# Kernel tuning notes

Hardware: AMD Instinct MI355X
Metric: run time of the kernel (lower is better)

## Reference

```python
import jax, jax.numpy as jnp
import numpy as np
from jax import lax

N_SECTIONS, N_CHANNELS = 8, 128
KT, KF = 32, 16                 # kernel (time, freq)
LPOST = 400                     # section_length_postsyn
LPRE = KT + LPOST - 1           # 431, section_length_presyn
SECTION_DISTANCE = 400          # LPRE - overlap (overlap = 31)
N_TIMESTEPS, FREQ = 3231, 256
THRESHOLD = 15.0


def setup_inputs() -> dict:
    key = jax.random.key(0)
    k1, k2 = jax.random.split(key)
    # scale so mean conv response ~ threshold (512 taps * 0.8 * mean(X))
    X = jax.random.uniform(k1, (N_TIMESTEPS, FREQ), dtype=jnp.float32) * 0.073
    # SpykeTorch Convolution init: N(0.8, 0.05)
    W = 0.8 + 0.05 * jax.random.normal(k2, (N_SECTIONS, N_CHANNELS, 1, KT, KF), dtype=jnp.float32)
    return {"X": X, "W": W}


def _sections(X):
    # [S, LPRE, FREQ] overlapping time windows
    starts = jnp.arange(N_SECTIONS) * SECTION_DISTANCE
    idx = starts[:, None] + jnp.arange(LPRE)
    return X[idx]


def _conv_sections(X, W):
    Xs = _sections(X)  # [S, LPRE, FREQ]
    def conv1(xs, w):
        # xs: [LPRE, FREQ], w: [C, 1, KT, KF] -> [C, LPOST, FOUT]
        return lax.conv_general_dilated(xs[None, None], w, (1, 1), 'VALID')[0]
    return jax.vmap(conv1)(Xs, W)  # [S, C, LPOST, FOUT]


def reference(X, W):
    pots = _conv_sections(X, W)                              # [S, C, 400, 241]
    # sf.fire: zero potentials < threshold, then sign -> binary spikes
    spikes = (pots >= THRESHOLD).astype(pots.dtype)
    # Pooling((LPOST, KF)): max-pool, stride = window, no padding
    pool = lax.reduce_window(spikes, -jnp.inf, lax.max,
                             (1, 1, LPOST, KF), (1, 1, LPOST, KF), 'VALID')  # [S, C, 1, 15]
    # sf.get_k_winners(pool): dim 0 (sections) acts as the time dimension
    T = pool.shape[0]
    spk = jnp.sign(pool)
    earliest = jnp.clip((T - spk.sum(axis=0)).astype(jnp.int32), 0, T - 1)   # [C,1,Fp]
    values = jnp.take_along_axis(pool, earliest[None], axis=0)[0]            # earliest spike value
    trunc = spk * values[None]
    v = trunc.max() * T
    trunc = trunc + spk * v
    total = trunc.sum(axis=0)                                # [C, 1, Fp]
    max_val = total.max()
    # winners[0][0] = feature (channel) index of the flat argmax
    feat = jnp.argmax(total.reshape(-1)) // (total.shape[1] * total.shape[2])
    return jnp.where(max_val != 0, feat, -1).astype(jnp.int32)
```

## Files before the change

kernel.cpp:

```cpp
#include <hip/hip_runtime.h>


using int2v  = __attribute__((ext_vector_type(2))) int;
using int4v  = __attribute__((ext_vector_type(4))) int;
using int8v  = __attribute__((ext_vector_type(8))) int;
using f32x8  = __attribute__((ext_vector_type(8))) float;
using f32x16 = __attribute__((ext_vector_type(16))) float;

#define SCALE_ONE 0x7F7F7F7F
#define THRESH_Q  4920.0f

#if __has_builtin(__builtin_amdgcn_cvt_scalef32_pk_fp4_f32)
#define HWFP4 1
#else
#define HWFP4 0
#endif

__device__ __forceinline__ unsigned f4enc(float v) {
  float r2 = __builtin_rintf(v + v);
  float r1 = __builtin_rintf(v);
  return (v <= 2.f) ? (unsigned)r2
       : (v <= 4.f) ? (unsigned)r1 + 2u
       : (v < 5.f)  ? 6u : 7u;
}

__device__ __forceinline__ unsigned pack8(f32x8 v) {
  unsigned d = 0;
#if HWFP4
  d = __builtin_amdgcn_cvt_scalef32_pk_fp4_f32(d, v[0], v[1], 1.0f, 0);
  d = __builtin_amdgcn_cvt_scalef32_pk_fp4_f32(d, v[2], v[3], 1.0f, 1);
  d = __builtin_amdgcn_cvt_scalef32_pk_fp4_f32(d, v[4], v[5], 1.0f, 2);
  d = __builtin_amdgcn_cvt_scalef32_pk_fp4_f32(d, v[6], v[7], 1.0f, 3);
#else
#pragma unroll
  for (int e = 0; e < 8; ++e) d |= f4enc(v[e]) << (4 * e);
#endif
  return d;
}

__global__ __launch_bounds__(256) void prep_kernel(const float* __restrict__ W,
                                                   unsigned char* __restrict__ Wp4,
                                                   int* __restrict__ pool) {
  int t = blockIdx.x * 256 + threadIdx.x;
  if (t < 15360) pool[t] = 0;
  int s = t >> 11, r = t & 2047, c = r >> 4, b = r & 15;
  const float* src = W + ((s * 128 + c) * 512 + b * 32);
  int4v o;
#pragma unroll
  for (int i = 0; i < 4; ++i) {
    f32x8 sv;
#pragma unroll
    for (int e = 0; e < 8; ++e) sv[e] = fmaxf(src[i * 8 + e], 0.f) * 4.f;
    o[i] = (int)pack8(sv);
  }
  *(int4v*)(Wp4 + s * 32768 + (b >> 1) * 4096 + (b & 1) * 2048 + c * 16) = o;
}

__global__ __launch_bounds__(512, 4) void conv_pool_kernel(const float* __restrict__ X,
                                                           const unsigned char* __restrict__ Wp4,
                                                           int* __restrict__ pool) {
  __shared__ __align__(16) unsigned char Ash[8 * 512];
  __shared__ __align__(16) unsigned char Bsh[32768];
  __shared__ unsigned poolbits[32];

  const int tid = threadIdx.x;
  const int bid = blockIdx.x;
  const int s   = bid / 390;
  const int rem = bid % 390;
  const int tt  = rem / 30;
  const int ft  = rem % 30;
  const int t0  = (tt == 12) ? 368 : tt * 32;
  const int fo0 = ft * 8, fp = ft >> 1;
  const int srow = s * 400 + t0;

  if (tid < 32) poolbits[tid] = 0;

  const int ok = tid < 504;
  const int it0 = ok ? tid : 0;
  const int d0 = it0 / 63, r0 = it0 % 63;
  const float* xs0 = X + (srow + r0) * 256 + fo0 + d0;
  f32x8 xv0a, xv0b;
#pragma unroll
  for (int e = 0; e < 8; ++e) {
    xv0a[e] = xs0[e];
    xv0b[e] = xs0[e + 8];
  }
  __builtin_amdgcn_sched_barrier(0);

  {
    const unsigned char* wbase = Wp4 + s * 32768;
#pragma unroll
    for (int it = 0; it < 4; ++it) {
      int off = (it * 512 + tid) * 16;
      __builtin_amdgcn_global_load_lds(
          (const __attribute__((address_space(1))) void*)(wbase + off),
          (__attribute__((address_space(3))) void*)(&Bsh[off]), 16, 0, 0);
    }
  }

  xv0a *= 82.f; xv0b *= 82.f;
  if (ok)
    *(int2v*)&Ash[d0 * 512 + r0 * 8] = (int2v){(int)pack8(xv0a), (int)pack8(xv0b)};

  const int w = tid >> 6, l = tid & 63;
  const int m31 = l & 31, ko = l >> 5;

  const int aoff = w * 512 + m31 * 8 + ko * 16;
  const int boff = ko * 2048 + m31 * 16;

  f32x16 acc[4];
#pragma unroll
  for (int b = 0; b < 4; ++b)
#pragma unroll
    for (int e = 0; e < 16; ++e) acc[b][e] = 0.f;

  __syncthreads();

#pragma unroll
  for (int ch = 0; ch < 8; ++ch) {
    int2v alo = *(const int2v*)&Ash[aoff + ch * 32];
    int2v ahi = *(const int2v*)&Ash[aoff + ch * 32 + 8];
    int8v Af = {alo[0], alo[1], ahi[0], ahi[1], 0, 0, 0, 0};
    const unsigned char* bb = Bsh + ch * 4096 + boff;
    int4v Bv[4];
    Bv[0] = *(const int4v*)(bb);
    Bv[1] = *(const int4v*)(bb + 512);
    Bv[2] = *(const int4v*)(bb + 1024);
    Bv[3] = *(const int4v*)(bb + 1536);
#pragma unroll
    for (int nt = 0; nt < 4; ++nt) {
      int8v Bf = {Bv[nt][0], Bv[nt][1], Bv[nt][2], Bv[nt][3], 0, 0, 0, 0};
      acc[nt] = __builtin_amdgcn_mfma_scale_f32_32x32x64_f8f6f4(
          Af, Bf, acc[nt], 4, 4, 0, SCALE_ONE, 0, SCALE_ONE);
    }
  }

  unsigned sp = 0;
#pragma unroll
  for (int nt = 0; nt < 4; ++nt) {
    float m0 = -1e30f;
#pragma unroll
    for (int e = 0; e < 16; ++e) m0 = fmaxf(m0, acc[nt][e]);
    if (m0 >= THRESH_Q) sp |= (1u << nt);
  }
  sp |= __shfl_xor(sp, 32, 64);
  if (l < 32 && sp) atomicOr(&poolbits[m31], sp);
  __syncthreads();

  if (tid < 128) {
    unsigned bits = poolbits[tid & 31];
    if ((bits >> (tid >> 5)) & 1)
      pool[(s * 128 + tid) * 15 + fp] = 1;
  }
}

__global__ __launch_bounds__(256) void winner_kernel(const int* __restrict__ pool,
                                                     float* __restrict__ out) {
  __shared__ int lp[15360];
  __shared__ int sh_v;
  __shared__ int sh_best;
  int tid = threadIdx.x;
  if (tid == 0) { sh_v = 0; sh_best = 0; }
  for (int i = tid; i < 15360; i += 256) lp[i] = pool[i];
  __syncthreads();

  int localv = 0;
  for (int p = tid; p < 1920; p += 256) {
    int c = p / 15, f = p % 15;
    int cnt = 0;
    for (int s = 0; s < 8; ++s) cnt += lp[(s * 128 + c) * 15 + f];
    if (cnt > 0) {
      int early = 8 - cnt; if (early > 7) early = 7;
      localv |= lp[(early * 128 + c) * 15 + f];
    }
  }
  if (localv) atomicOr(&sh_v, 1);
  __syncthreads();

  const int v = sh_v * 8;
  int localbest = 0;
  for (int p = tid; p < 1920; p += 256) {
    int c = p / 15, f = p % 15;
    int cnt = 0;
    for (int s = 0; s < 8; ++s) cnt += lp[(s * 128 + c) * 15 + f];
    int early = 8 - cnt; if (early > 7) early = 7;
    int val = lp[(early * 128 + c) * 15 + f];
    int total = cnt * (val + v);
    int pack = (total << 12) | (4095 - p);
    if (pack > localbest) localbest = pack;
  }
  atomicMax(&sh_best, localbest);
  __syncthreads();

  if (tid == 0) {
    int total = sh_best >> 12;
    int p = 4095 - (sh_best & 4095);
    int feat = p / 15;
    out[0] = (total != 0) ? (float)feat : -1.0f;
  }
}

extern "C" void kernel_launch(void* const* d_in, const int* in_sizes, int n_in,
                              void* d_out, int out_size, void* d_ws, size_t ws_size,
                              hipStream_t stream) {
  (void)in_sizes; (void)n_in; (void)out_size; (void)ws_size;
  const float* X = (const float*)d_in[0];
  const float* W = (const float*)d_in[1];
  unsigned char* Wp4 = (unsigned char*)d_ws;
  int* pool = (int*)((char*)d_ws + (1 << 18));

  prep_kernel<<<64, 256, 0, stream>>>(W, Wp4, pool);
  conv_pool_kernel<<<3120, 512, 0, stream>>>(X, Wp4, pool);
  winner_kernel<<<1, 256, 0, stream>>>(pool, (float*)d_out);
}
```

Baseline: 90.64 us.

## Make conv blocks persistent per section with double-buffered input tiles

The conv kernel drops from 3120 one-tile blocks to 512 persistent blocks, each pinned to one section and handling 6-7 tiles. The section's packed FP4 weights are loaded into LDS once per block instead of once per tile. The next tile's X is prefetched and packed into a second LDS buffer while the current tile's MFMAs run, and pool bits are double-buffered too. This cuts redundant weight traffic and launch/prologue overhead, but gives fewer blocks, which can hurt occupancy and load balance.

```diff
diff --git a/kernel.cpp b/kernel.cpp
--- a/kernel.cpp
+++ b/kernel.cpp
@@ -59,31 +59,29 @@
 __global__ __launch_bounds__(512, 4) void conv_pool_kernel(const float* __restrict__ X,
                                                            const unsigned char* __restrict__ Wp4,
                                                            int* __restrict__ pool) {
-  __shared__ __align__(16) unsigned char Ash[8 * 512];
+  __shared__ __align__(16) unsigned char Ash[2][8 * 512];
   __shared__ __align__(16) unsigned char Bsh[32768];
-  __shared__ unsigned poolbits[32];
+  __shared__ unsigned poolbits[2][32];
 
   const int tid = threadIdx.x;
-  const int bid = blockIdx.x;
-  const int s   = bid / 390;
-  const int rem = bid % 390;
-  const int tt  = rem / 30;
-  const int ft  = rem % 30;
-  const int t0  = (tt == 12) ? 368 : tt * 32;
-  const int fo0 = ft * 8, fp = ft >> 1;
-  const int srow = s * 400 + t0;
-
-  if (tid < 32) poolbits[tid] = 0;
-
-  const int ok = tid < 504;
+  const int s   = blockIdx.x & 7;
+  const int lb  = blockIdx.x >> 3;
+  const int NT  = (lb < 6) ? 7 : 6;
+
+  const int ok  = tid < 504;
   const int it0 = ok ? tid : 0;
-  const int d0 = it0 / 63, r0 = it0 % 63;
-  const float* xs0 = X + (srow + r0) * 256 + fo0 + d0;
-  f32x8 xv0a, xv0b;
-#pragma unroll
-  for (int e = 0; e < 8; ++e) {
-    xv0a[e] = xs0[e];
-    xv0b[e] = xs0[e + 8];
+  const int d0  = it0 / 63, r0 = it0 % 63;
+  const float* Xs = X + (s * 400 + r0) * 256 + d0;
+
+  if (tid < 64) poolbits[tid >> 5][tid & 31] = 0;
+
+  f32x8 xa, xb;
+  {
+    int tau = lb, tt = tau / 30, ft = tau % 30;
+    int t0 = (tt == 12) ? 368 : tt * 32;
+    const float* xp = Xs + t0 * 256 + ft * 8;
+#pragma unroll
+    for (int e = 0; e < 8; ++e) { xa[e] = xp[e]; xb[e] = xp[e + 8]; }
   }
   __builtin_amdgcn_sched_barrier(0);
 
@@ -98,59 +96,89 @@
     }
   }
 
-  xv0a *= 82.f; xv0b *= 82.f;
-  if (ok)
-    *(int2v*)&Ash[d0 * 512 + r0 * 8] = (int2v){(int)pack8(xv0a), (int)pack8(xv0b)};
+  xa *= 82.f; xb *= 82.f;
+  if (ok) *(int2v*)&Ash[0][d0 * 512 + r0 * 8] = (int2v){(int)pack8(xa), (int)pack8(xb)};
+  if (NT > 1) {
+    int tau = lb + 64, tt = tau / 30, ft = tau % 30;
+    int t0 = (tt == 12) ? 368 : tt * 32;
+    const float* xp = Xs + t0 * 256 + ft * 8;
+#pragma unroll
+    for (int e = 0; e < 8; ++e) { xa[e] = xp[e]; xb[e] = xp[e + 8]; }
+  }
+  __syncthreads();
 
   const int w = tid >> 6, l = tid & 63;
   const int m31 = l & 31, ko = l >> 5;
-
   const int aoff = w * 512 + m31 * 8 + ko * 16;
   const int boff = ko * 2048 + m31 * 16;
 
-  f32x16 acc[4];
-#pragma unroll
-  for (int b = 0; b < 4; ++b)
-#pragma unroll
-    for (int e = 0; e < 16; ++e) acc[b][e] = 0.f;
-
-  __syncthreads();
-
-#pragma unroll
-  for (int ch = 0; ch < 8; ++ch) {
-    int2v alo = *(const int2v*)&Ash[aoff + ch * 32];
-    int2v ahi = *(const int2v*)&Ash[aoff + ch * 32 + 8];
-    int8v Af = {alo[0], alo[1], ahi[0], ahi[1], 0, 0, 0, 0};
-    const unsigned char* bb = Bsh + ch * 4096 + boff;
-    int4v Bv[4];
-    Bv[0] = *(const int4v*)(bb);
-    Bv[1] = *(const int4v*)(bb + 512);
-    Bv[2] = *(const int4v*)(bb + 1024);
-    Bv[3] = *(const int4v*)(bb + 1536);
+#pragma unroll 1
+  for (int i = 0; i < NT; ++i) {
+    const unsigned char* ab = &Ash[i & 1][0];
+
+    f32x16 acc[4];
+#pragma unroll
+    for (int b = 0; b < 4; ++b)
+#pragma unroll
+      for (int e = 0; e < 16; ++e) acc[b][e] = 0.f;
+#pragma unroll
+    for (int ch = 0; ch < 8; ++ch) {
+      int2v alo = *(const int2v*)&ab[aoff + ch * 32];
+      int2v ahi = *(const int2v*)&ab[aoff + ch * 32 + 8];
+      int8v Af = {alo[0], alo[1], ahi[0], ahi[1], 0, 0, 0, 0};
+      const unsigned char* bb = Bsh + ch * 4096 + boff;
+      int4v Bv[4];
+      Bv[0] = *(const int4v*)(bb);
+      Bv[1] = *(const int4v*)(bb + 512);
+      Bv[2] = *(const int4v*)(bb + 1024);
+      Bv[3] = *(const int4v*)(bb + 1536);
+#pragma unroll
+      for (int nt = 0; nt < 4; ++nt) {
+        int8v Bf = {Bv[nt][0], Bv[nt][1], Bv[nt][2], Bv[nt][3], 0, 0, 0, 0};
+        acc[nt] = __builtin_amdgcn_mfma_scale_f32_32x32x64_f8f6f4(
+            Af, Bf, acc[nt], 4, 4, 0, SCALE_ONE, 0, SCALE_ONE);
+      }
+    }
+
+    unsigned sp = 0;
 #pragma unroll
     for (int nt = 0; nt < 4; ++nt) {
-      int8v Bf = {Bv[nt][0], Bv[nt][1], Bv[nt][2], Bv[nt][3], 0, 0, 0, 0};
-      acc[nt] = __builtin_amdgcn_mfma_scale_f32_32x32x64_f8f6f4(
-          Af, Bf, acc[nt], 4, 4, 0, SCALE_ONE, 0, SCALE_ONE);
-    }
-  }
-
-  unsigned sp = 0;
-#pragma unroll
-  for (int nt = 0; nt < 4; ++nt) {
-    float m0 = -1e30f;
-#pragma unroll
-    for (int e = 0; e < 16; ++e) m0 = fmaxf(m0, acc[nt][e]);
-    if (m0 >= THRESH_Q) sp |= (1u << nt);
-  }
-  sp |= __shfl_xor(sp, 32, 64);
-  if (l < 32 && sp) atomicOr(&poolbits[m31], sp);
-  __syncthreads();
-
-  if (tid < 128) {
-    unsigned bits = poolbits[tid & 31];
-    if ((bits >> (tid >> 5)) & 1)
-      pool[(s * 128 + tid) * 15 + fp] = 1;
+      float m0 = -1e30f;
+#pragma unroll
+      for (int e = 0; e < 16; ++e) m0 = fmaxf(m0, acc[nt][e]);
+      if (m0 >= THRESH_Q) sp |= (1u << nt);
+    }
+    sp |= __shfl_xor(sp, 32, 64);
+    if (l < 32 && sp) atomicOr(&poolbits[i & 1][m31], sp);
+
+    if (i + 1 < NT) {
+      xa *= 82.f; xb *= 82.f;
+      if (ok)
+        *(int2v*)&Ash[(i + 1) & 1][d0 * 512 + r0 * 8] =
+            (int2v){(int)pack8(xa), (int)pack8(xb)};
+      if (i + 2 < NT) {
+        int tau = lb + 64 * (i + 2), tt = tau / 30, ft = tau % 30;
+        int t0 = (tt == 12) ? 368 : tt * 32;
+        const float* xp = Xs + t0 * 256 + ft * 8;
+#pragma unroll
+        for (int e = 0; e < 8; ++e) { xa[e] = xp[e]; xb[e] = xp[e + 8]; }
+      }
+    }
+
+    __syncthreads();
+
+    if (tid < 32) {
+      unsigned bits = poolbits[i & 1][tid];
+      poolbits[i & 1][tid] = 0;
+      if (bits) {
+        int tau = lb + 64 * i;
+        int fp = (tau % 30) >> 1;
+#pragma unroll
+        for (int nt = 0; nt < 4; ++nt)
+          if ((bits >> nt) & 1)
+            pool[(s * 128 + nt * 32 + tid) * 15 + fp] = 1;
+      }
+    }
   }
 }
 
@@ -210,6 +238,6 @@
   int* pool = (int*)((char*)d_ws + (1 << 18));
 
   prep_kernel<<<64, 256, 0, stream>>>(W, Wp4, pool);
-  conv_pool_kernel<<<3120, 512, 0, stream>>>(X, Wp4, pool);
+  conv_pool_kernel<<<512, 512, 0, stream>>>(X, Wp4, pool);
   winner_kernel<<<1, 256, 0, stream>>>(pool, (float*)d_out);
 }
```

Measured after the change: 86.73 us. 1.05x faster.
